# Performance work log

Measured on AMD Instinct MI355X. Metric: run time of the kernel, lower is better.

The kernel has to match this reference:

```python
import jax, jax.numpy as jnp
import numpy as np

B, N, DIM = 4, 1024, 1024
HEADS, DH = 16, 64
INNER = HEADS * DH          # 1024
PROJ_H = max(16, DH // 8)   # 16
TOP_K = 256
TEMP = 1.0
SCALE = DH ** -0.5
LN_EPS = 1e-5


def setup_inputs() -> dict:
    key = jax.random.key(0)
    ks = jax.random.split(key, 9)
    s = 0.02
    return {
        "x": jax.random.normal(ks[0], (B, N, DIM), dtype=jnp.float32),
        "w_qkv": jax.random.normal(ks[1], (3 * INNER, DIM), dtype=jnp.float32) * s,
        "w_out": jax.random.normal(ks[2], (DIM, INNER), dtype=jnp.float32) * s,
        "b_out": jnp.zeros((DIM,), dtype=jnp.float32),
        "ln_g": jnp.ones((DH,), dtype=jnp.float32),
        "ln_b": jnp.zeros((DH,), dtype=jnp.float32),
        "w1": jax.random.normal(ks[3], (PROJ_H, DH), dtype=jnp.float32) * s,
        "b1": jnp.zeros((PROJ_H,), dtype=jnp.float32),
        "w2": jax.random.normal(ks[4], (1, PROJ_H), dtype=jnp.float32) * s,
        "b2": jnp.zeros((1,), dtype=jnp.float32),
    }


def _soma_gate(token_feat, ln_g, ln_b, w1, b1, w2, b2):
    # token_feat: [B, N, DH] -> gate [B, N] in (0,1)
    mu = token_feat.mean(axis=-1, keepdims=True)
    var = token_feat.var(axis=-1, keepdims=True)
    H = (token_feat - mu) * jax.lax.rsqrt(var + LN_EPS) * ln_g + ln_b
    h = jax.nn.gelu(H @ w1.T + b1, approximate=False)
    scores = (h @ w2.T + b2)[..., 0]                       # [B, N]
    scores = scores / (TEMP + 1e-12)
    # top-k soft mask: non-topk positions set to -1e9 before sigmoid
    topk_vals, topk_idx = jax.lax.top_k(scores, TOP_K)
    b_idx = jnp.arange(scores.shape[0])[:, None]
    scores = jnp.full_like(scores, -1e9).at[b_idx, topk_idx].set(topk_vals)
    return jax.nn.sigmoid(scores)


def reference(x, w_qkv, w_out, b_out, ln_g, ln_b, w1, b1, w2, b2):
    Bx, Nx, _ = x.shape
    qkv = x @ w_qkv.T                                      # [B, N, 3*INNER]
    q, k, v = jnp.split(qkv, 3, axis=-1)
    to_heads = lambda t: t.reshape(Bx, Nx, HEADS, DH).transpose(0, 2, 1, 3)
    q, k, v = to_heads(q), to_heads(k), to_heads(v)        # [B, H, N, DH]

    dots = jnp.einsum('bhid,bhjd->bhij', q, k) * SCALE     # [B, H, N, N]

    q_mean = q.mean(axis=1)                                # [B, N, DH]
    gate = _soma_gate(q_mean, ln_g, ln_b, w1, b1, w2, b2)  # [B, N]
    dots = dots * (gate[:, None, :, None] * gate[:, None, None, :])

    attn = jax.nn.softmax(dots, axis=-1)
    out = jnp.einsum('bhij,bhjd->bhid', attn, v)           # [B, H, N, DH]
    out = out.transpose(0, 2, 1, 3).reshape(Bx, Nx, INNER)
    return out @ w_out.T + b_out
```

## Files before the change

kernel.cpp:

```cpp
#include <hip/hip_runtime.h>
#include <hip/hip_bf16.h>
#include <stdint.h>

typedef __bf16 bf16;
typedef __bf16 bf16x8 __attribute__((ext_vector_type(8)));
typedef float floatx4 __attribute__((ext_vector_type(4)));

typedef const __attribute__((address_space(1))) uint32_t glb_u32;
typedef __attribute__((address_space(3))) uint32_t lds_u32;

__device__ __forceinline__ void cp16(void* lds, const void* gp) {
    __builtin_amdgcn_global_load_lds((glb_u32*)gp, (lds_u32*)lds, 16, 0, 0);
}

#define MFMA16(a, b, c) __builtin_amdgcn_mfma_f32_16x16x32_bf16((a), (b), (c), 0, 0, 0)
#define SCALE_ 0.125f

__global__ __launch_bounds__(256) void k_cvt_prep(
    const float* __restrict__ x, const float* __restrict__ wq,
    const float* __restrict__ wo, bf16* __restrict__ xb,
    bf16* __restrict__ xl, bf16* __restrict__ wqb, bf16* __restrict__ wob,
    bf16* __restrict__ whl, float* __restrict__ xsum) {
    __shared__ float red[4][64];
    if (blockIdx.x < 4096) {
        size_t i8 = ((size_t)blockIdx.x * 256 + threadIdx.x) * 8;
        const float* src; bf16* dst; size_t off; bool isx = false;
        if (i8 < 4194304)      { src = x;  dst = xb;  off = i8; isx = true; }
        else if (i8 < 7340032) { src = wq; dst = wqb; off = i8 - 4194304; }
        else                   { src = wo; dst = wob; off = i8 - 7340032; }
        float4 a = *(const float4*)(src + off);
        float4 b = *(const float4*)(src + off + 4);
        union { bf16 h[8]; uint4 u; } hi, lo;
        hi.h[0] = (bf16)a.x; hi.h[1] = (bf16)a.y; hi.h[2] = (bf16)a.z; hi.h[3] = (bf16)a.w;
        hi.h[4] = (bf16)b.x; hi.h[5] = (bf16)b.y; hi.h[6] = (bf16)b.z; hi.h[7] = (bf16)b.w;
        *(uint4*)(dst + off) = hi.u;
        if (isx) {
            lo.h[0] = (bf16)(a.x - (float)hi.h[0]);
            lo.h[1] = (bf16)(a.y - (float)hi.h[1]);
            lo.h[2] = (bf16)(a.z - (float)hi.h[2]);
            lo.h[3] = (bf16)(a.w - (float)hi.h[3]);
            lo.h[4] = (bf16)(b.x - (float)hi.h[4]);
            lo.h[5] = (bf16)(b.y - (float)hi.h[5]);
            lo.h[6] = (bf16)(b.z - (float)hi.h[6]);
            lo.h[7] = (bf16)(b.w - (float)hi.h[7]);
            *(uint4*)(xl + off) = lo.u;
        }
    } else if (blockIdx.x < 4352) {
        int t = (blockIdx.x - 4096) * 256 + threadIdx.x;
        int k = t & 1023, d = t >> 10;
        float s = 0.f;
        #pragma unroll
        for (int h = 0; h < 16; ++h) s += wq[(size_t)(h * 64 + d) * 1024 + k];
        s *= (1.f / 16.f);
        bf16 hi = (bf16)s;
        whl[(size_t)d * 1024 + k] = hi;
        whl[(size_t)(64 + d) * 1024 + k] = (bf16)(s - (float)hi);
    } else {
        int j = blockIdx.x - 4352;
        int b = j >> 4, c0 = (j & 15) << 6;
        int lane = threadIdx.x & 63, q = threadIdx.x >> 6;
        const float* p = x + (size_t)b * 1048576 + (size_t)q * 262144 + c0 + lane;
        float s = 0.f;
        #pragma unroll 8
        for (int n = 0; n < 256; ++n) s += p[(size_t)n * 1024];
        red[q][lane] = s;
        __syncthreads();
        if (threadIdx.x < 64)
            xsum[b * 1024 + c0 + threadIdx.x] =
                red[0][threadIdx.x] + red[1][threadIdx.x] +
                red[2][threadIdx.x] + red[3][threadIdx.x];
    }
}

__global__ __launch_bounds__(256) void k_score_gemm(
    const bf16* __restrict__ xh, const bf16* __restrict__ xl,
    const bf16* __restrict__ whl, float* __restrict__ qm8) {
    __shared__ bf16 Ah[64 * 32];
    __shared__ bf16 Al[64 * 32];
    __shared__ bf16 Bs[128 * 32];
    const int t = threadIdx.x;
    const int lane = t & 63;
    const int w = t >> 6;
    const int m0 = (blockIdx.x >> 3) * 64;
    const int kbase = (blockIdx.x & 7) * 128;
    const int srow = t >> 2;
    const int scol = (t & 3) * 8;
    const int fr = lane & 15;
    const int kc = (lane >> 4) * 8;

    floatx4 zero4 = {0.f, 0.f, 0.f, 0.f};
    floatx4 acc[4] = {zero4, zero4, zero4, zero4};

    for (int k0 = kbase; k0 < kbase + 128; k0 += 32) {
        __syncthreads();
        cp16(Ah + t * 8,        xh + (size_t)(m0 + srow) * 1024 + k0 + scol);
        cp16(Al + t * 8,        xl + (size_t)(m0 + srow) * 1024 + k0 + scol);
        cp16(Bs + t * 8,        whl + (size_t)srow * 1024 + k0 + scol);
        cp16(Bs + t * 8 + 2048, whl + (size_t)(srow + 64) * 1024 + k0 + scol);
        __syncthreads();
        bf16x8 ah, al, bh[4], bl[4];
        ah = *(const bf16x8*)&Ah[(w * 16 + fr) * 32 + kc];
        al = *(const bf16x8*)&Al[(w * 16 + fr) * 32 + kc];
        #pragma unroll
        for (int ni = 0; ni < 4; ++ni) {
            bh[ni] = *(const bf16x8*)&Bs[(ni * 16 + fr) * 32 + kc];
            bl[ni] = *(const bf16x8*)&Bs[(64 + ni * 16 + fr) * 32 + kc];
        }
        #pragma unroll
        for (int ni = 0; ni < 4; ++ni) {
            acc[ni] = MFMA16(ah, bh[ni], acc[ni]);
            acc[ni] = MFMA16(ah, bl[ni], acc[ni]);
            acc[ni] = MFMA16(al, bh[ni], acc[ni]);
        }
    }

    const int rowb = (lane >> 4) * 4;
    const size_t kofs = (size_t)(blockIdx.x & 7) * 4096;
    #pragma unroll
    for (int ni = 0; ni < 4; ++ni)
        #pragma unroll
        for (int r = 0; r < 4; ++r)
            qm8[(kofs + m0 + w * 16 + rowb + r) * 64 + ni * 16 + fr] = acc[ni][r];
}

__global__ __launch_bounds__(256) void k_score_tail(
    const float* __restrict__ qm8, const float* __restrict__ lng,
    const float* __restrict__ lnb, const float* __restrict__ w1f,
    const float* __restrict__ b1f, const float* __restrict__ w2f,
    const float* __restrict__ b2f, float* __restrict__ scores) {
    const int w = threadIdx.x >> 6, lane = threadIdx.x & 63;
    const int r = blockIdx.x * 4 + w;
    __shared__ float Hs[4][64];
    __shared__ float hh[4][16];

    float qm = 0.f;
    #pragma unroll
    for (int ks = 0; ks < 8; ++ks)
        qm += qm8[((size_t)ks * 4096 + r) * 64 + lane];
    float s = qm;
    #pragma unroll
    for (int off = 32; off > 0; off >>= 1) s += __shfl_xor(s, off);
    float mu = s * (1.f / 64.f);
    float dx = qm - mu;
    float v2 = dx * dx;
    #pragma unroll
    for (int off = 32; off > 0; off >>= 1) v2 += __shfl_xor(v2, off);
    float var = v2 * (1.f / 64.f);
    float H = dx * (1.0f / sqrtf(var + 1e-5f)) * lng[lane] + lnb[lane];
    Hs[w][lane] = H;
    if (lane < 16) {
        float a = b1f[lane];
        #pragma unroll
        for (int d = 0; d < 64; ++d) a += Hs[w][d] * w1f[lane * 64 + d];
        hh[w][lane] = 0.5f * a * (1.0f + erff(a * 0.70710678118654752f));
    }
    if (lane == 0) {
        float sc = b2f[0];
        #pragma unroll
        for (int p = 0; p < 16; ++p) sc += hh[w][p] * w2f[p];
        scores[r] = sc;
    }
}

__global__ __launch_bounds__(256) void k_topk(const float* __restrict__ scores,
                                              float* __restrict__ gate,
                                              int* __restrict__ idx,
                                              float* __restrict__ gsel) {
    const int w = threadIdx.x >> 6, lane = threadIdx.x & 63;
    const float* sc = scores + w * 1024;
    float s[16];
    uint32_t key[16];
    #pragma unroll
    for (int i = 0; i < 16; ++i) {
        s[i] = sc[lane * 16 + i];
        uint32_t u = __float_as_uint(s[i]);
        key[i] = (u >> 31) ? ~u : (u | 0x80000000u);
    }
    uint32_t prefix = 0;
    for (int bit = 31; bit >= 0; --bit) {
        uint32_t cand = prefix | (1u << bit);
        int c = 0;
        #pragma unroll
        for (int i = 0; i < 16; ++i) c += (key[i] >= cand);
        #pragma unroll
        for (int off = 1; off < 64; off <<= 1) c += __shfl_xor(c, off);
        if (c >= 256) prefix = cand;
    }
    int cg = 0, eq = 0;
    #pragma unroll
    for (int i = 0; i < 16; ++i) { cg += (key[i] > prefix); eq += (key[i] == prefix); }
    #pragma unroll
    for (int off = 1; off < 64; off <<= 1) cg += __shfl_xor(cg, off);
    const int quota = 256 - cg;
    int xs = eq;
    #pragma unroll
    for (int off = 1; off < 64; off <<= 1) {
        int y = __shfl_up(xs, off);
        if (lane >= off) xs += y;
    }
    int run = xs - eq;
    bool selv[16];
    int cnt = 0;
    #pragma unroll
    for (int i = 0; i < 16; ++i) {
        bool sel = key[i] > prefix;
        if (key[i] == prefix) { sel = (run < quota); run++; }
        selv[i] = sel;
        cnt += sel ? 1 : 0;
        gate[w * 1024 + lane * 16 + i] = sel ? 1.0f / (1.0f + expf(-s[i])) : 0.0f;
    }
    int xc = cnt;
    #pragma unroll
    for (int off = 1; off < 64; off <<= 1) {
        int y = __shfl_up(xc, off);
        if (lane >= off) xc += y;
    }
    int pos = xc - cnt;
    #pragma unroll
    for (int i = 0; i < 16; ++i) {
        if (selv[i]) {
            idx[w * 256 + pos]  = lane * 16 + i;
            gsel[w * 256 + pos] = 1.0f / (1.0f + expf(-s[i]));
            pos++;
        }
    }
}

__global__ __launch_bounds__(256) void k_qkv_sel(
    const bf16* __restrict__ xb, const bf16* __restrict__ wqb,
    const int* __restrict__ idx, bf16* __restrict__ qsel,
    bf16* __restrict__ ksel, bf16* __restrict__ VselT,
    const float* __restrict__ xsum, float* __restrict__ meanVbuf) {
    __shared__ bf16 As[128 * 32];
    __shared__ bf16 Bs[128 * 32];
    __shared__ float xsS[1024];
    const int t = threadIdx.x;

    if (blockIdx.x >= 192) {
        const int j = blockIdx.x - 192, b = j >> 2, kq = j & 3;
        for (int k = t; k < 1024; k += 256) xsS[k] = xsum[b * 1024 + k];
        __syncthreads();
        const int k2 = kq * 256 + t;
        const bf16* wr = wqb + (size_t)(2048 + k2) * 1024;
        float s = 0.f;
        for (int k = 0; k < 1024; k += 8) {
            bf16x8 v = *(const bf16x8*)(wr + k);
            #pragma unroll
            for (int jj = 0; jj < 8; ++jj) s += (float)v[jj] * xsS[k + jj];
        }
        meanVbuf[b * 1024 + k2] = s * (1.f / 1024.f);
        return;
    }

    const int lane = t & 63;
    const int w = t >> 6;
    const int srow = t >> 2;
    const int scol = (t & 3) * 8;
    const int wm = (w & 1) * 64;
    const int wn = (w >> 1) * 64;
    const int fr = lane & 15;
    const int kc = (lane >> 4) * 8;

    const int bid = blockIdx.x;
    const int n0 = (bid % 24) * 128;
    const int m0 = (bid / 24) * 128;
    const bf16* Bsrc = wqb + (size_t)n0 * 1024;
    const int mg1 = m0 + srow, mg2 = mg1 + 64;
    const int tok1 = idx[(mg1 >> 8) * 256 + (mg1 & 255)];
    const int tok2 = idx[(mg2 >> 8) * 256 + (mg2 & 255)];
    const size_t abase1 = ((size_t)(mg1 >> 8) * 1024 + tok1) * 1024;
    const size_t abase2 = ((size_t)(mg2 >> 8) * 1024 + tok2) * 1024;

    floatx4 zero4 = {0.f, 0.f, 0.f, 0.f};
    floatx4 acc[4][4];
    #pragma unroll
    for (int i = 0; i < 4; ++i)
        #pragma unroll
        for (int j = 0; j < 4; ++j) acc[i][j] = zero4;

    for (int k0 = 0; k0 < 1024; k0 += 32) {
        __syncthreads();
        cp16(As + t * 8,        xb + abase1 + k0 + scol);
        cp16(As + t * 8 + 2048, xb + abase2 + k0 + scol);
        cp16(Bs + t * 8,        Bsrc + (size_t)srow * 1024 + k0 + scol);
        cp16(Bs + t * 8 + 2048, Bsrc + (size_t)(srow + 64) * 1024 + k0 + scol);
        __syncthreads();
        bf16x8 a[4], b[4];
        #pragma unroll
        for (int mi = 0; mi < 4; ++mi)
            a[mi] = *(const bf16x8*)&As[(wm + mi * 16 + fr) * 32 + kc];
        #pragma unroll
        for (int ni = 0; ni < 4; ++ni)
            b[ni] = *(const bf16x8*)&Bs[(wn + ni * 16 + fr) * 32 + kc];
        #pragma unroll
        for (int mi = 0; mi < 4; ++mi)
            #pragma unroll
            for (int ni = 0; ni < 4; ++ni)
                acc[mi][ni] = MFMA16(a[mi], b[ni], acc[mi][ni]);
    }

    const int rowb = (lane >> 4) * 4;
    #pragma unroll
    for (int ni = 0; ni < 4; ++ni) {
        const int n_base = n0 + wn + ni * 16;
        const int region = n_base >> 10;
        const int nn = n_base & 1023;
        const int h = nn >> 6;
        const int dd = (nn & 63) + fr;
        if (region < 2) {
            #pragma unroll
            for (int mi = 0; mi < 4; ++mi)
                #pragma unroll
                for (int r = 0; r < 4; ++r) {
                    const int mg = m0 + wm + mi * 16 + rowb + r;
                    const bf16 v = (bf16)acc[mi][ni][r];
                    if (region == 0) {
                        qsel[(size_t)mg * 1024 + h * 64 + dd] = v;
                    } else {
                        const int b = mg >> 8, s = mg & 255;
                        ksel[(((size_t)(b * 16 + h)) * 256 + s) * 64 + dd] = v;
                    }
                }
        } else {
            #pragma unroll
            for (int mi = 0; mi < 4; ++mi) {
                const int mgb = m0 + wm + mi * 16 + rowb;
                const int b = mgb >> 8, s0 = mgb & 255;
                union { bf16 h4[4]; uint2 u; } pk;
                #pragma unroll
                for (int r = 0; r < 4; ++r) pk.h4[r] = (bf16)acc[mi][ni][r];
                *(uint2*)&VselT[(((size_t)(b * 16 + h)) * 64 + dd) * 256 + s0] = pk.u;
            }
        }
    }
}

__global__ __launch_bounds__(256) void k_attn(
    bf16* __restrict__ qsel, const bf16* __restrict__ Ksel,
    const bf16* __restrict__ VselT, const float* __restrict__ gsel,
    const float* __restrict__ meanVbuf, const bf16* __restrict__ wob,
    const float* __restrict__ b_out, float* __restrict__ ubase) {
    __shared__ bf16 Qs[64 * 72];
    __shared__ bf16 Ks[64 * 72];
    __shared__ bf16 Vs[64 * 72];
    __shared__ bf16 Ps[4][16 * 72];
    __shared__ float redS[4][64];
    __shared__ float SumV[64];
    __shared__ float mvS[1024];
    const int t = threadIdx.x;

    if (blockIdx.x >= 256) {
        const int j = blockIdx.x - 256, bb = j >> 2, nq = j & 3;
        for (int k = t; k < 1024; k += 256) mvS[k] = meanVbuf[bb * 1024 + k];
        __syncthreads();
        const int n = nq * 256 + t;
        const bf16* wr = wob + (size_t)n * 1024;
        float s = b_out[n];
        for (int k = 0; k < 1024; k += 8) {
            bf16x8 v = *(const bf16x8*)(wr + k);
            #pragma unroll
            for (int jj = 0; jj < 8; ++jj) s += (float)v[jj] * mvS[k + jj];
        }
        ubase[bb * 1024 + n] = s;
        return;
    }

    const int bh = blockIdx.x >> 2;
    const int qt = blockIdx.x & 3;
    const int b = bh >> 4, h = bh & 15;
    const int w = t >> 6, lane = t & 63;
    const int m0 = qt * 64;
    const bf16* kb = Ksel + (size_t)bh * 16384;
    const bf16* vb = VselT + (size_t)bh * 16384;

    #pragma unroll
    for (int c = 0; c < 2; ++c) {
        int idx2 = t + 256 * c, row = idx2 >> 3, c8 = (idx2 & 7) * 8;
        *(uint4*)&Qs[row * 72 + c8] =
            *(const uint4*)&qsel[(size_t)(b * 256 + m0 + row) * 1024 + h * 64 + c8];
    }
    {
        const int dd_ = t & 63, pp_ = t >> 6;
        const bf16* vr = vb + (size_t)dd_ * 256 + pp_ * 64;
        float ss = 0.f;
        #pragma unroll
        for (int k = 0; k < 64; k += 8) {
            bf16x8 v = *(const bf16x8*)(vr + k);
            #pragma unroll
            for (int jj = 0; jj < 8; ++jj) ss += (float)v[jj];
        }
        redS[pp_][dd_] = ss;
    }
    const int fr = lane & 15;
    const int kq = lane >> 4;
    const int rowb = kq * 4;
    __syncthreads();
    if (t < 64)
        SumV[t] = meanVbuf[b * 1024 + h * 64 + t] * 1024.f -
                  (redS[0][t] + redS[1][t] + redS[2][t] + redS[3][t]);
    bf16x8 aq[2];
    aq[0] = *(const bf16x8*)&Qs[(w * 16 + fr) * 72 + kq * 8];
    aq[1] = *(const bf16x8*)&Qs[(w * 16 + fr) * 72 + 32 + kq * 8];

    float gq[4];
    #pragma unroll
    for (int r = 0; r < 4; ++r)
        gq[r] = gsel[b * 256 + m0 + w * 16 + rowb + r] * SCALE_;

    float mrow[4] = {0.f, 0.f, 0.f, 0.f};
    float lrow[4] = {0.f, 0.f, 0.f, 0.f};
    floatx4 zero4 = {0.f, 0.f, 0.f, 0.f};
    floatx4 Of[4] = {zero4, zero4, zero4, zero4};

    for (int jt = 0; jt < 4; ++jt) {
        const int j0 = jt * 64;
        __syncthreads();
        #pragma unroll
        for (int c = 0; c < 2; ++c) {
            int idx2 = t + 256 * c, row = idx2 >> 3, c8 = (idx2 & 7) * 8;
            *(uint4*)&Ks[row * 72 + c8] = *(const uint4*)&kb[(size_t)(j0 + row) * 64 + c8];
            *(uint4*)&Vs[row * 72 + c8] = *(const uint4*)&vb[(size_t)row * 256 + j0 + c8];
        }
        __syncthreads();

        floatx4 S[4] = {zero4, zero4, zero4, zero4};
        #pragma unroll
        for (int ks = 0; ks < 2; ++ks) {
            #pragma unroll
            for (int ni = 0; ni < 4; ++ni) {
                bf16x8 bfr = *(const bf16x8*)&Ks[(ni * 16 + fr) * 72 + ks * 32 + kq * 8];
                S[ni] = MFMA16(aq[ks], bfr, S[ni]);
            }
        }
        float gk[4];
        #pragma unroll
        for (int ni = 0; ni < 4; ++ni) gk[ni] = gsel[b * 256 + j0 + ni * 16 + fr];

        float p[4][4], rmax[4] = {0.f, 0.f, 0.f, 0.f};
        #pragma unroll
        for (int ni = 0; ni < 4; ++ni)
            #pragma unroll
            for (int r = 0; r < 4; ++r) {
                float sv = S[ni][r] * (gq[r] * gk[ni]);
                p[ni][r] = sv;
                rmax[r] = fmaxf(rmax[r], sv);
            }
        #pragma unroll
        for (int r = 0; r < 4; ++r) {
            #pragma unroll
            for (int off = 1; off < 16; off <<= 1)
                rmax[r] = fmaxf(rmax[r], __shfl_xor(rmax[r], off));
        }
        float alpha[4], rsum[4] = {0.f, 0.f, 0.f, 0.f};
        #pragma unroll
        for (int r = 0; r < 4; ++r) {
            float mn = fmaxf(mrow[r], rmax[r]);
            alpha[r] = __expf(mrow[r] - mn);
            mrow[r] = mn;
        }
        #pragma unroll
        for (int ni = 0; ni < 4; ++ni)
            #pragma unroll
            for (int r = 0; r < 4; ++r) {
                float pv = __expf(p[ni][r] - mrow[r]);
                p[ni][r] = pv;
                rsum[r] += pv;
            }
        #pragma unroll
        for (int r = 0; r < 4; ++r) {
            #pragma unroll
            for (int off = 1; off < 16; off <<= 1) rsum[r] += __shfl_xor(rsum[r], off);
            lrow[r] = lrow[r] * alpha[r] + rsum[r];
        }
        #pragma unroll
        for (int nd = 0; nd < 4; ++nd)
            #pragma unroll
            for (int r = 0; r < 4; ++r) Of[nd][r] *= alpha[r];

        #pragma unroll
        for (int ni = 0; ni < 4; ++ni)
            #pragma unroll
            for (int r = 0; r < 4; ++r)
                Ps[w][(rowb + r) * 72 + ni * 16 + fr] = (bf16)p[ni][r];

        #pragma unroll
        for (int ks = 0; ks < 2; ++ks) {
            bf16x8 ap = *(const bf16x8*)&Ps[w][fr * 72 + ks * 32 + kq * 8];
            #pragma unroll
            for (int nd = 0; nd < 4; ++nd) {
                bf16x8 bv = *(const bf16x8*)&Vs[(nd * 16 + fr) * 72 + ks * 32 + kq * 8];
                Of[nd] = MFMA16(ap, bv, Of[nd]);
            }
        }
    }

    #pragma unroll
    for (int nd = 0; nd < 4; ++nd)
        #pragma unroll
        for (int r = 0; r < 4; ++r) {
            float em = __expf(-mrow[r]);
            float num = Of[nd][r] + em * SumV[nd * 16 + fr];
            float den = lrow[r] + 768.0f * em;
            qsel[(size_t)(b * 256 + m0 + w * 16 + rowb + r) * 1024 +
                 h * 64 + nd * 16 + fr] = (bf16)(num / den);
        }
}

__global__ __launch_bounds__(256) void k_out_sel(
    const bf16* __restrict__ A, const bf16* __restrict__ wob,
    const float* __restrict__ b_out, const int* __restrict__ idx,
    const float* __restrict__ ubase, const float* __restrict__ gate,
    float* __restrict__ out) {
    __shared__ bf16 As[128 * 32];
    __shared__ bf16 Bs[128 * 32];
    const int t = threadIdx.x;
    const int gb = blockIdx.x;

    if (gb >= 64) {
        const int fb = gb - 64;
        const int c = t * 4;
        #pragma unroll
        for (int r = 0; r < 4; ++r) {
            const int tokg = fb * 4 + r;
            if (gate[tokg] > 0.f) continue;
            const int b = tokg >> 10;
            *(float4*)(out + (size_t)tokg * 1024 + c) =
                *(const float4*)(ubase + b * 1024 + c);
        }
        return;
    }

    const int lane = t & 63;
    const int w = t >> 6;
    const int n0 = (gb & 7) * 128;
    const int m0 = (gb >> 3) * 128;
    const bf16* Bsrc = wob + (size_t)n0 * 1024;

    const int srow = t >> 2;
    const int scol = (t & 3) * 8;
    const int wm = (w & 1) * 64;
    const int wn = (w >> 1) * 64;
    const int fr = lane & 15;
    const int kc = (lane >> 4) * 8;

    floatx4 zero4 = {0.f, 0.f, 0.f, 0.f};
    floatx4 acc[4][4];
    #pragma unroll
    for (int i = 0; i < 4; ++i)
        #pragma unroll
        for (int j = 0; j < 4; ++j) acc[i][j] = zero4;

    for (int k0 = 0; k0 < 1024; k0 += 32) {
        __syncthreads();
        cp16(As + t * 8,        A + (size_t)(m0 + srow) * 1024 + k0 + scol);
        cp16(As + t * 8 + 2048, A + (size_t)(m0 + srow + 64) * 1024 + k0 + scol);
        cp16(Bs + t * 8,        Bsrc + (size_t)srow * 1024 + k0 + scol);
        cp16(Bs + t * 8 + 2048, Bsrc + (size_t)(srow + 64) * 1024 + k0 + scol);
        __syncthreads();
        bf16x8 a[4], b[4];
        #pragma unroll
        for (int mi = 0; mi < 4; ++mi)
            a[mi] = *(const bf16x8*)&As[(wm + mi * 16 + fr) * 32 + kc];
        #pragma unroll
        for (int ni = 0; ni < 4; ++ni)
            b[ni] = *(const bf16x8*)&Bs[(wn + ni * 16 + fr) * 32 + kc];
        #pragma unroll
        for (int mi = 0; mi < 4; ++mi)
            #pragma unroll
            for (int ni = 0; ni < 4; ++ni)
                acc[mi][ni] = MFMA16(a[mi], b[ni], acc[mi][ni]);
    }

    const int rowb = (lane >> 4) * 4;
    #pragma unroll
    for (int ni = 0; ni < 4; ++ni) {
        const int ng = n0 + wn + ni * 16 + fr;
        const float bias = b_out[ng];
        #pragma unroll
        for (int mi = 0; mi < 4; ++mi)
            #pragma unroll
            for (int r = 0; r < 4; ++r) {
                const int mg = m0 + wm + mi * 16 + rowb + r;
                const float val = acc[mi][ni][r] + bias;
                const int bb = mg >> 8, ss = mg & 255;
                const int tok = idx[bb * 256 + ss];
                out[((size_t)bb * 1024 + tok) * 1024 + ng] = val;
            }
    }
}

extern "C" void kernel_launch(void* const* d_in, const int* in_sizes, int n_in,
                              void* d_out, int out_size, void* d_ws, size_t ws_size,
                              hipStream_t stream) {
    const float* x     = (const float*)d_in[0];
    const float* w_qkv = (const float*)d_in[1];
    const float* w_out = (const float*)d_in[2];
    const float* b_out = (const float*)d_in[3];
    const float* ln_g  = (const float*)d_in[4];
    const float* ln_b  = (const float*)d_in[5];
    const float* w1    = (const float*)d_in[6];
    const float* b1    = (const float*)d_in[7];
    const float* w2    = (const float*)d_in[8];
    const float* b2    = (const float*)d_in[9];
    float* out = (float*)d_out;

    char* ws = (char*)d_ws;
    bf16*  qsel  = (bf16*)(ws);
    bf16*  ksel  = (bf16*)(ws + 4194304);
    bf16*  VselT = (bf16*)(ws + 6291456);
    float* qm8   = (float*)(ws);
    float* xsum  = (float*)(ws + 8388608);
    bf16*  xb    = (bf16*)(ws + 16777216);
    bf16*  wqb   = (bf16*)(ws + 25165824);
    bf16*  wob   = (bf16*)(ws + 31457280);
    int*   idx      = (int*)(ws + 33554432);
    float* gsel     = (float*)(ws + 33558528);
    float* scores   = (float*)(ws + 33562624);
    float* gate     = (float*)(ws + 33579008);
    float* meanVbuf = (float*)(ws + 33595392);
    float* ubase    = (float*)(ws + 33611776);
    bf16*  whl      = (bf16*)(ws + 33685504);
    bf16*  xlbuf    = (bf16*)(ws + 35651584);

    k_cvt_prep<<<4416, 256, 0, stream>>>(x, w_qkv, w_out, xb, xlbuf, wqb, wob, whl, xsum);
    k_score_gemm<<<512, 256, 0, stream>>>(xb, xlbuf, whl, qm8);
    k_score_tail<<<1024, 256, 0, stream>>>(qm8, ln_g, ln_b, w1, b1, w2, b2, scores);
    k_topk<<<1, 256, 0, stream>>>(scores, gate, idx, gsel);
    k_qkv_sel<<<208, 256, 0, stream>>>(xb, wqb, idx, qsel, ksel, VselT, xsum, meanVbuf);
    k_attn<<<272, 256, 0, stream>>>(qsel, ksel, VselT, gsel, meanVbuf, wob, b_out, ubase);
    k_out_sel<<<1088, 256, 0, stream>>>(qsel, wob, b_out, idx, ubase, gate, out);
}
```

Baseline: 201.7 us.

## Shrink QKV GEMM tiles and split-K the output projection for more blocks

The selected-token QKV GEMM drops from 128x128 to 64x128 tiles, doubling its block count from 192 to 384 so more of the device's compute units are occupied. The output projection becomes a split-K (two halves) GEMM with 64x128 tiles writing fp32 partials into reused workspace, followed by a separate reduction kernel that adds the halves and bias, scatters rows to their token positions and fills the non-selected tokens. This targets low occupancy on small GEMMs (1024 selected rows), at the cost of extra partial-sum traffic, one more launch, and lower per-block data reuse.

```diff
diff --git a/kernel.cpp b/kernel.cpp
--- a/kernel.cpp
+++ b/kernel.cpp
@@ -231,13 +231,13 @@
     const int* __restrict__ idx, bf16* __restrict__ qsel,
     bf16* __restrict__ ksel, bf16* __restrict__ VselT,
     const float* __restrict__ xsum, float* __restrict__ meanVbuf) {
-    __shared__ bf16 As[128 * 32];
+    __shared__ bf16 As[64 * 32];
     __shared__ bf16 Bs[128 * 32];
     __shared__ float xsS[1024];
     const int t = threadIdx.x;
 
-    if (blockIdx.x >= 192) {
-        const int j = blockIdx.x - 192, b = j >> 2, kq = j & 3;
+    if (blockIdx.x >= 384) {
+        const int j = blockIdx.x - 384, b = j >> 2, kq = j & 3;
         for (int k = t; k < 1024; k += 256) xsS[k] = xsum[b * 1024 + k];
         __syncthreads();
         const int k2 = kq * 256 + t;
@@ -256,53 +256,48 @@
     const int w = t >> 6;
     const int srow = t >> 2;
     const int scol = (t & 3) * 8;
-    const int wm = (w & 1) * 64;
-    const int wn = (w >> 1) * 64;
     const int fr = lane & 15;
     const int kc = (lane >> 4) * 8;
 
     const int bid = blockIdx.x;
     const int n0 = (bid % 24) * 128;
-    const int m0 = (bid / 24) * 128;
+    const int m0 = (bid / 24) * 64;
     const bf16* Bsrc = wqb + (size_t)n0 * 1024;
-    const int mg1 = m0 + srow, mg2 = mg1 + 64;
+    const int mg1 = m0 + srow;
     const int tok1 = idx[(mg1 >> 8) * 256 + (mg1 & 255)];
-    const int tok2 = idx[(mg2 >> 8) * 256 + (mg2 & 255)];
     const size_t abase1 = ((size_t)(mg1 >> 8) * 1024 + tok1) * 1024;
-    const size_t abase2 = ((size_t)(mg2 >> 8) * 1024 + tok2) * 1024;
 
     floatx4 zero4 = {0.f, 0.f, 0.f, 0.f};
-    floatx4 acc[4][4];
+    floatx4 acc[4][2];
     #pragma unroll
     for (int i = 0; i < 4; ++i)
         #pragma unroll
-        for (int j = 0; j < 4; ++j) acc[i][j] = zero4;
+        for (int j = 0; j < 2; ++j) acc[i][j] = zero4;
 
     for (int k0 = 0; k0 < 1024; k0 += 32) {
         __syncthreads();
         cp16(As + t * 8,        xb + abase1 + k0 + scol);
-        cp16(As + t * 8 + 2048, xb + abase2 + k0 + scol);
         cp16(Bs + t * 8,        Bsrc + (size_t)srow * 1024 + k0 + scol);
         cp16(Bs + t * 8 + 2048, Bsrc + (size_t)(srow + 64) * 1024 + k0 + scol);
         __syncthreads();
-        bf16x8 a[4], b[4];
+        bf16x8 a[4], b[2];
         #pragma unroll
         for (int mi = 0; mi < 4; ++mi)
-            a[mi] = *(const bf16x8*)&As[(wm + mi * 16 + fr) * 32 + kc];
-        #pragma unroll
-        for (int ni = 0; ni < 4; ++ni)
-            b[ni] = *(const bf16x8*)&Bs[(wn + ni * 16 + fr) * 32 + kc];
+            a[mi] = *(const bf16x8*)&As[(mi * 16 + fr) * 32 + kc];
+        #pragma unroll
+        for (int ni = 0; ni < 2; ++ni)
+            b[ni] = *(const bf16x8*)&Bs[(w * 32 + ni * 16 + fr) * 32 + kc];
         #pragma unroll
         for (int mi = 0; mi < 4; ++mi)
             #pragma unroll
-            for (int ni = 0; ni < 4; ++ni)
+            for (int ni = 0; ni < 2; ++ni)
                 acc[mi][ni] = MFMA16(a[mi], b[ni], acc[mi][ni]);
     }
 
     const int rowb = (lane >> 4) * 4;
     #pragma unroll
-    for (int ni = 0; ni < 4; ++ni) {
-        const int n_base = n0 + wn + ni * 16;
+    for (int ni = 0; ni < 2; ++ni) {
+        const int n_base = n0 + w * 32 + ni * 16;
         const int region = n_base >> 10;
         const int nn = n_base & 1023;
         const int h = nn >> 6;
@@ -312,7 +307,7 @@
             for (int mi = 0; mi < 4; ++mi)
                 #pragma unroll
                 for (int r = 0; r < 4; ++r) {
-                    const int mg = m0 + wm + mi * 16 + rowb + r;
+                    const int mg = m0 + mi * 16 + rowb + r;
                     const bf16 v = (bf16)acc[mi][ni][r];
                     if (region == 0) {
                         qsel[(size_t)mg * 1024 + h * 64 + dd] = v;
@@ -324,7 +319,7 @@
         } else {
             #pragma unroll
             for (int mi = 0; mi < 4; ++mi) {
-                const int mgb = m0 + wm + mi * 16 + rowb;
+                const int mgb = m0 + mi * 16 + rowb;
                 const int b = mgb >> 8, s0 = mgb & 255;
                 union { bf16 h4[4]; uint2 u; } pk;
                 #pragma unroll
@@ -506,18 +501,89 @@
         }
 }
 
-__global__ __launch_bounds__(256) void k_out_sel(
+__global__ __launch_bounds__(256) void k_out_gemm(
     const bf16* __restrict__ A, const bf16* __restrict__ wob,
-    const float* __restrict__ b_out, const int* __restrict__ idx,
-    const float* __restrict__ ubase, const float* __restrict__ gate,
-    float* __restrict__ out) {
-    __shared__ bf16 As[128 * 32];
+    float* __restrict__ outP) {
+    __shared__ bf16 As[64 * 32];
     __shared__ bf16 Bs[128 * 32];
     const int t = threadIdx.x;
-    const int gb = blockIdx.x;
-
-    if (gb >= 64) {
-        const int fb = gb - 64;
+    const int lane = t & 63;
+    const int w = t >> 6;
+    const int srow = t >> 2;
+    const int scol = (t & 3) * 8;
+    const int fr = lane & 15;
+    const int kc = (lane >> 4) * 8;
+
+    const int ks = blockIdx.x >> 7;
+    const int rem = blockIdx.x & 127;
+    const int m0 = (rem >> 3) * 64;
+    const int n0 = (rem & 7) * 128;
+    const int kbase = ks * 512;
+    const bf16* Bsrc = wob + (size_t)n0 * 1024;
+
+    floatx4 zero4 = {0.f, 0.f, 0.f, 0.f};
+    floatx4 acc[4][2];
+    #pragma unroll
+    for (int i = 0; i < 4; ++i)
+        #pragma unroll
+        for (int j = 0; j < 2; ++j) acc[i][j] = zero4;
+
+    for (int k0 = kbase; k0 < kbase + 512; k0 += 32) {
+        __syncthreads();
+        cp16(As + t * 8,        A + (size_t)(m0 + srow) * 1024 + k0 + scol);
+        cp16(Bs + t * 8,        Bsrc + (size_t)srow * 1024 + k0 + scol);
+        cp16(Bs + t * 8 + 2048, Bsrc + (size_t)(srow + 64) * 1024 + k0 + scol);
+        __syncthreads();
+        bf16x8 a[4], b[2];
+        #pragma unroll
+        for (int mi = 0; mi < 4; ++mi)
+            a[mi] = *(const bf16x8*)&As[(mi * 16 + fr) * 32 + kc];
+        #pragma unroll
+        for (int ni = 0; ni < 2; ++ni)
+            b[ni] = *(const bf16x8*)&Bs[(w * 32 + ni * 16 + fr) * 32 + kc];
+        #pragma unroll
+        for (int mi = 0; mi < 4; ++mi)
+            #pragma unroll
+            for (int ni = 0; ni < 2; ++ni)
+                acc[mi][ni] = MFMA16(a[mi], b[ni], acc[mi][ni]);
+    }
+
+    const int rowb = (lane >> 4) * 4;
+    float* dst = outP + (size_t)ks * 1048576;
+    #pragma unroll
+    for (int ni = 0; ni < 2; ++ni) {
+        const int ng = n0 + w * 32 + ni * 16 + fr;
+        #pragma unroll
+        for (int mi = 0; mi < 4; ++mi)
+            #pragma unroll
+            for (int r = 0; r < 4; ++r) {
+                const int mg = m0 + mi * 16 + rowb + r;
+                dst[(size_t)mg * 1024 + ng] = acc[mi][ni][r];
+            }
+    }
+}
+
+__global__ __launch_bounds__(256) void k_out_red(
+    const float* __restrict__ outP, const float* __restrict__ b_out,
+    const int* __restrict__ idx, const float* __restrict__ ubase,
+    const float* __restrict__ gate, float* __restrict__ out) {
+    const int t = threadIdx.x, gb = blockIdx.x;
+    if (gb < 1024) {
+        const int mg = gb;
+        const int c = t * 4;
+        float4 v0 = *(const float4*)(outP + (size_t)mg * 1024 + c);
+        float4 v1 = *(const float4*)(outP + 1048576 + (size_t)mg * 1024 + c);
+        float4 bb = *(const float4*)(b_out + c);
+        float4 r;
+        r.x = v0.x + v1.x + bb.x;
+        r.y = v0.y + v1.y + bb.y;
+        r.z = v0.z + v1.z + bb.z;
+        r.w = v0.w + v1.w + bb.w;
+        const int b = mg >> 8, s = mg & 255;
+        const int tok = idx[b * 256 + s];
+        *(float4*)(out + ((size_t)b * 1024 + tok) * 1024 + c) = r;
+    } else {
+        const int fb = gb - 1024;
         const int c = t * 4;
         #pragma unroll
         for (int r = 0; r < 4; ++r) {
@@ -527,65 +593,6 @@
             *(float4*)(out + (size_t)tokg * 1024 + c) =
                 *(const float4*)(ubase + b * 1024 + c);
         }
-        return;
-    }
-
-    const int lane = t & 63;
-    const int w = t >> 6;
-    const int n0 = (gb & 7) * 128;
-    const int m0 = (gb >> 3) * 128;
-    const bf16* Bsrc = wob + (size_t)n0 * 1024;
-
-    const int srow = t >> 2;
-    const int scol = (t & 3) * 8;
-    const int wm = (w & 1) * 64;
-    const int wn = (w >> 1) * 64;
-    const int fr = lane & 15;
-    const int kc = (lane >> 4) * 8;
-
-    floatx4 zero4 = {0.f, 0.f, 0.f, 0.f};
-    floatx4 acc[4][4];
-    #pragma unroll
-    for (int i = 0; i < 4; ++i)
-        #pragma unroll
-        for (int j = 0; j < 4; ++j) acc[i][j] = zero4;
-
-    for (int k0 = 0; k0 < 1024; k0 += 32) {
-        __syncthreads();
-        cp16(As + t * 8,        A + (size_t)(m0 + srow) * 1024 + k0 + scol);
-        cp16(As + t * 8 + 2048, A + (size_t)(m0 + srow + 64) * 1024 + k0 + scol);
-        cp16(Bs + t * 8,        Bsrc + (size_t)srow * 1024 + k0 + scol);
-        cp16(Bs + t * 8 + 2048, Bsrc + (size_t)(srow + 64) * 1024 + k0 + scol);
-        __syncthreads();
-        bf16x8 a[4], b[4];
-        #pragma unroll
-        for (int mi = 0; mi < 4; ++mi)
-            a[mi] = *(const bf16x8*)&As[(wm + mi * 16 + fr) * 32 + kc];
-        #pragma unroll
-        for (int ni = 0; ni < 4; ++ni)
-            b[ni] = *(const bf16x8*)&Bs[(wn + ni * 16 + fr) * 32 + kc];
-        #pragma unroll
-        for (int mi = 0; mi < 4; ++mi)
-            #pragma unroll
-            for (int ni = 0; ni < 4; ++ni)
-                acc[mi][ni] = MFMA16(a[mi], b[ni], acc[mi][ni]);
-    }
-
-    const int rowb = (lane >> 4) * 4;
-    #pragma unroll
-    for (int ni = 0; ni < 4; ++ni) {
-        const int ng = n0 + wn + ni * 16 + fr;
-        const float bias = b_out[ng];
-        #pragma unroll
-        for (int mi = 0; mi < 4; ++mi)
-            #pragma unroll
-            for (int r = 0; r < 4; ++r) {
-                const int mg = m0 + wm + mi * 16 + rowb + r;
-                const float val = acc[mi][ni][r] + bias;
-                const int bb = mg >> 8, ss = mg & 255;
-                const int tok = idx[bb * 256 + ss];
-                out[((size_t)bb * 1024 + tok) * 1024 + ng] = val;
-            }
     }
 }
 
@@ -611,6 +618,7 @@
     float* qm8   = (float*)(ws);
     float* xsum  = (float*)(ws + 8388608);
     bf16*  xb    = (bf16*)(ws + 16777216);
+    float* outP  = (float*)(ws + 16777216);
     bf16*  wqb   = (bf16*)(ws + 25165824);
     bf16*  wob   = (bf16*)(ws + 31457280);
     int*   idx      = (int*)(ws + 33554432);
@@ -626,7 +634,8 @@
     k_score_gemm<<<512, 256, 0, stream>>>(xb, xlbuf, whl, qm8);
     k_score_tail<<<1024, 256, 0, stream>>>(qm8, ln_g, ln_b, w1, b1, w2, b2, scores);
     k_topk<<<1, 256, 0, stream>>>(scores, gate, idx, gsel);
-    k_qkv_sel<<<208, 256, 0, stream>>>(xb, wqb, idx, qsel, ksel, VselT, xsum, meanVbuf);
+    k_qkv_sel<<<400, 256, 0, stream>>>(xb, wqb, idx, qsel, ksel, VselT, xsum, meanVbuf);
     k_attn<<<272, 256, 0, stream>>>(qsel, ksel, VselT, gsel, meanVbuf, wob, b_out, ubase);
-    k_out_sel<<<1088, 256, 0, stream>>>(qsel, wob, b_out, idx, ubase, gate, out);
-}
+    k_out_gemm<<<256, 256, 0, stream>>>(qsel, wob, outP);
+    k_out_red<<<2048, 256, 0, stream>>>(outP, b_out, idx, ubase, gate, out);
+}
```

Result: no change. 198.8 us (median of 2 runs) (-1.4%).
